# Kernel optimization log

Hardware: AMD Instinct MI355X
Metric: run time of the kernel (lower is better)

The kernel has to match this reference:

```python
import jax, jax.numpy as jnp
import numpy as np
import math

N, LQ, C = 4, 5440, 256
H, L, P = 8, 4, 4
D = C // H
SHAPES = [(64, 64), (32, 32), (16, 16), (8, 8)]
STARTS = [0, 4096, 5120, 5376]
LEN_IN = 5440


def setup_inputs() -> dict:
    key = jax.random.key(0)
    ks = jax.random.split(key, 12)
    s = 1.0 / math.sqrt(C)
    return {
        "query": jax.random.normal(ks[0], (N, LQ, C), jnp.float32),
        "reference_points": jax.random.uniform(ks[1], (N, LQ, L, 2), jnp.float32),
        "input_flatten": jax.random.normal(ks[2], (N, LEN_IN, C), jnp.float32),
        "input_spatial_shapes": jnp.asarray(SHAPES, jnp.int32),
        "input_level_start_index": jnp.asarray(STARTS, jnp.int32),
        "w_off": jax.random.normal(ks[3], (C, H * L * P * 2), jnp.float32) * 0.01,
        "b_off": jax.random.normal(ks[4], (H * L * P * 2,), jnp.float32) * 0.5,
        "w_attn": jax.random.normal(ks[5], (C, H * L * P), jnp.float32) * 0.01,
        "b_attn": jnp.zeros((H * L * P,), jnp.float32),
        "w_val": jax.random.normal(ks[6], (C, C), jnp.float32) * s,
        "b_val": jnp.zeros((C,), jnp.float32),
        "w_out": jax.random.normal(ks[7], (C, C), jnp.float32) * s,
        "b_out": jnp.zeros((C,), jnp.float32),
    }


def _gather_corner(lv, yi, xi, w):
    # lv: (N, h*w, H, D); yi, xi: (N, Lq, H, P) int32 -> (N, Lq, H, P, D)
    n, lq, h_, p_ = yi.shape
    idx = yi * w + xi
    idx2 = idx.transpose(0, 1, 3, 2).reshape(n, lq * p_, h_)[..., None]
    g = jnp.take_along_axis(lv, idx2, axis=1)  # (N, Lq*P, H, D)
    return g.reshape(n, lq, p_, h_, -1).transpose(0, 1, 3, 2, 4)


def _msdeform(query, reference_points, input_flatten, shapes, starts,
              w_off, b_off, w_attn, b_attn, w_val, b_val, w_out, b_out):
    n, lq, c = query.shape
    value = (input_flatten @ w_val + b_val).reshape(n, -1, H, D)
    off = (query @ w_off + b_off).reshape(n, lq, H, L, P, 2)
    attn = jax.nn.softmax((query @ w_attn + b_attn).reshape(n, lq, H, L * P), axis=-1)
    # sampling locations in [0,1], (N, Lq, H, L, P, 2)
    loc = jnp.clip(reference_points[:, :, None, :, None, :] + off, 0.0, 1.0)
    sampled = []
    for lvl, (hh, ww) in enumerate(shapes):
        s0 = starts[lvl]
        lv = value[:, s0:s0 + hh * ww]  # (N, hh*ww, H, D)
        xy = loc[:, :, :, lvl] * jnp.asarray([ww, hh], jnp.float32) - 0.5  # (N,Lq,H,P,2)
        x, y = xy[..., 0], xy[..., 1]
        x0 = jnp.floor(x)
        y0 = jnp.floor(y)
        x0i = jnp.clip(x0.astype(jnp.int32), 0, ww - 1)
        x1i = jnp.clip(x0.astype(jnp.int32) + 1, 0, ww - 1)
        y0i = jnp.clip(y0.astype(jnp.int32), 0, hh - 1)
        y1i = jnp.clip(y0.astype(jnp.int32) + 1, 0, hh - 1)
        x0f, x1f = x0i.astype(x.dtype), x1i.astype(x.dtype)
        y0f, y1f = y0i.astype(y.dtype), y1i.astype(y.dtype)
        wa = ((x1f - x) * (y1f - y))[..., None]
        wb = ((x1f - x) * (y - y0f))[..., None]
        wc = ((x - x0f) * (y1f - y))[..., None]
        wd = ((x - x0f) * (y - y0f))[..., None]
        va = _gather_corner(lv, y0i, x0i, ww)
        vb = _gather_corner(lv, y1i, x0i, ww)
        vc = _gather_corner(lv, y0i, x1i, ww)
        vd = _gather_corner(lv, y1i, x1i, ww)
        sampled.append(wa * va + wb * vb + wc * vc + wd * vd)
    sampled = jnp.concatenate(sampled, axis=3)  # (N, Lq, H, L*P, D)
    out = jnp.einsum('nqhp,nqhpd->nqhd', attn, sampled).reshape(n, lq, c)
    return out @ w_out + b_out


def reference(query, reference_points, input_flatten, input_spatial_shapes,
              input_level_start_index, w_off, b_off, w_attn, b_attn,
              w_val, b_val, w_out, b_out):
    shapes = [tuple(int(v) for v in row) for row in np.asarray(input_spatial_shapes)]
    starts = [int(v) for v in np.asarray(input_level_start_index)]
    return _msdeform(query, reference_points, input_flatten, shapes, starts,
                     w_off, b_off, w_attn, b_attn, w_val, b_val, w_out, b_out)
```

## Files before the change

kernel.cpp:

```cpp
#include <hip/hip_runtime.h>
#include <hip/hip_fp16.h>
#include <math.h>

#define C_DIM 256
#define H_DIM 8
#define L_DIM 4
#define P_DIM 4
#define LQ 5440
#define LEN_IN 5440
#define NB 4
#define M_ROWS (NB * LQ)
#define NPANEL (M_ROWS / 128)

typedef __attribute__((ext_vector_type(8))) _Float16 f16x8;
typedef __attribute__((ext_vector_type(8))) unsigned short u16x8;
typedef __attribute__((ext_vector_type(4))) float f32x4;

__device__ __forceinline__ void split_f32(float a, __half& h, __half& l) {
    h = __float2half(a);
    l = __float2half(a - __half2float(h));
}

__global__ __launch_bounds__(256) void convert_all(const float* __restrict__ w_val,
                                                   const float* __restrict__ w_off,
                                                   const float* __restrict__ w_attn,
                                                   const float* __restrict__ w_out,
                                                   const float* __restrict__ b_off,
                                                   const float* __restrict__ b_attn,
                                                   __half* __restrict__ wv_hi, __half* __restrict__ wv_lo,
                                                   __half* __restrict__ wc_hi, __half* __restrict__ wc_lo,
                                                   __half* __restrict__ wt_hi, __half* __restrict__ wt_lo,
                                                   float* __restrict__ bc) {
    const int b = blockIdx.x, k = threadIdx.x;
    if (b < 896) {
        const float* w; __half *hi, *lo; int ncols, col, orow;
        if (b < 256)      { w = w_val;  hi = wv_hi; lo = wv_lo; ncols = 256; col = b;       orow = col; }
        else if (b < 512) { w = w_off;  hi = wc_hi; lo = wc_lo; ncols = 256; col = b - 256; orow = col; }
        else if (b < 640) { w = w_attn; hi = wc_hi; lo = wc_lo; ncols = 128; col = b - 512; orow = col + 256; }
        else              { w = w_out;  hi = wt_hi; lo = wt_lo; ncols = 256; col = b - 640; orow = col; }
        const float a = w[(size_t)k * ncols + col];
        __half h, l;
        split_f32(a, h, l);
        hi[(size_t)orow * 256 + k] = h;
        lo[(size_t)orow * 256 + k] = l;
    } else if (b == 896) {
        bc[k] = b_off[k];
    } else {
        if (k < 128) bc[256 + k] = b_attn[k];
    }
}

template <int NC, int BN, int MINW>
__global__ __launch_bounds__(256, MINW) void gemm_f16x3(const float* __restrict__ A,
                                                        const __half* __restrict__ Bhi,
                                                        const __half* __restrict__ Blo,
                                                        const float* __restrict__ bias,
                                                        float* __restrict__ outp) {
    constexpr int NF = BN / 32;
    constexpr int BCH = BN / 64;
    constexpr int WC = BN / 2;
    constexpr int NCH = WC / 4;

    __shared__ __align__(16) __half sA[2][128][32];
    __shared__ __align__(16) __half sB[2][BN][32];
    __shared__ __align__(16) float sepi[4][16][WC];

    const int n0 = blockIdx.x * BN;
    const int row0 = blockIdx.y * 128;
    const int t = threadIdx.x;
    const int w = t >> 6, lane = t & 63;
    const int bm = (w >> 1) * 64, bn = (w & 1) * WC;
    const int fr = lane & 15;
    const int fc = lane >> 4;

    const int ar1 = t >> 2, ar2 = ar1 + 64;
    const int ak8 = t & 3;
    const int asw1 = (ak8 ^ ((ar1 >> 1) & 3)) * 8;
    const int asw2 = (ak8 ^ ((ar2 >> 1) & 3)) * 8;
    const int bc8 = t & 3;
    int brr[BCH], bsw[BCH];
#pragma unroll
    for (int cc = 0; cc < BCH; ++cc) {
        brr[cc] = (t >> 2) + 64 * cc;
        bsw[cc] = (bc8 ^ ((brr[cc] >> 1) & 3)) * 8;
    }

    const size_t ga1 = (size_t)(row0 + ar1) * 256 + ak8 * 8;
    const size_t ga2 = (size_t)(row0 + ar2) * 256 + ak8 * 8;
    size_t gb[BCH];
#pragma unroll
    for (int cc = 0; cc < BCH; ++cc) gb[cc] = (size_t)(n0 + brr[cc]) * 256 + bc8 * 8;

    f32x4 acc[4][NF];
#pragma unroll
    for (int m = 0; m < 4; ++m)
#pragma unroll
        for (int n = 0; n < NF; ++n)
#pragma unroll
            for (int r = 0; r < 4; ++r) acc[m][n][r] = 0.f;

    float4 pa[4];
    float4 pb[2 * BCH];
    pa[0] = *(const float4*)(A + ga1);
    pa[1] = *(const float4*)(A + ga1 + 4);
    pa[2] = *(const float4*)(A + ga2);
    pa[3] = *(const float4*)(A + ga2 + 4);
#pragma unroll
    for (int cc = 0; cc < BCH; ++cc) {
        pb[cc] = *(const float4*)(Bhi + gb[cc]);
        pb[BCH + cc] = *(const float4*)(Blo + gb[cc]);
    }

    for (int kt = 0; kt < 8; ++kt) {
        if (kt) __syncthreads();
#pragma unroll
        for (int ch = 0; ch < 2; ++ch) {
            const float4 u = pa[2 * ch], v = pa[2 * ch + 1];
            const float e[8] = {u.x, u.y, u.z, u.w, v.x, v.y, v.z, v.w};
            u16x8 Hh, Ll;
#pragma unroll
            for (int i = 0; i < 8; ++i) {
                __half h, l;
                split_f32(e[i], h, l);
                Hh[i] = __half_as_ushort(h);
                Ll[i] = __half_as_ushort(l);
            }
            const int row = ch ? ar2 : ar1;
            const int sw = ch ? asw2 : asw1;
            *(u16x8*)&sA[0][row][sw] = Hh;
            *(u16x8*)&sA[1][row][sw] = Ll;
        }
#pragma unroll
        for (int cc = 0; cc < BCH; ++cc) {
            *(float4*)&sB[0][brr[cc]][bsw[cc]] = pb[cc];
            *(float4*)&sB[1][brr[cc]][bsw[cc]] = pb[BCH + cc];
        }
        __syncthreads();
        if (kt < 7) {
            const size_t ko = (size_t)(kt + 1) * 32;
            pa[0] = *(const float4*)(A + ga1 + ko);
            pa[1] = *(const float4*)(A + ga1 + ko + 4);
            pa[2] = *(const float4*)(A + ga2 + ko);
            pa[3] = *(const float4*)(A + ga2 + ko + 4);
#pragma unroll
            for (int cc = 0; cc < BCH; ++cc) {
                pb[cc] = *(const float4*)(Bhi + gb[cc] + ko);
                pb[BCH + cc] = *(const float4*)(Blo + gb[cc] + ko);
            }
        }

        f16x8 bhf[NF], blf[NF];
#pragma unroll
        for (int n = 0; n < NF; ++n) {
            const int rowb = bn + n * 16 + fr;
            const int swb = (fc ^ ((rowb >> 1) & 3)) * 8;
            bhf[n] = *(const f16x8*)&sB[0][rowb][swb];
            blf[n] = *(const f16x8*)&sB[1][rowb][swb];
        }
#pragma unroll
        for (int m = 0; m < 4; ++m) {
            const int rowa = bm + m * 16 + fr;
            const int swa = (fc ^ ((rowa >> 1) & 3)) * 8;
            const f16x8 ah = *(const f16x8*)&sA[0][rowa][swa];
            const f16x8 al = *(const f16x8*)&sA[1][rowa][swa];
#pragma unroll
            for (int n = 0; n < NF; ++n) {
                acc[m][n] = __builtin_amdgcn_mfma_f32_16x16x32_f16(ah, bhf[n], acc[m][n], 0, 0, 0);
                acc[m][n] = __builtin_amdgcn_mfma_f32_16x16x32_f16(al, bhf[n], acc[m][n], 0, 0, 0);
                acc[m][n] = __builtin_amdgcn_mfma_f32_16x16x32_f16(ah, blf[n], acc[m][n], 0, 0, 0);
            }
        }
    }

    float bv[NF];
#pragma unroll
    for (int n = 0; n < NF; ++n) bv[n] = bias[n0 + bn + n * 16 + fr];

#pragma unroll
    for (int m = 0; m < 4; ++m) {
#pragma unroll
        for (int n = 0; n < NF; ++n) {
            const int kch = n * 4 + (fr >> 2);
            const int lo4 = fr & 3;
#pragma unroll
            for (int r = 0; r < 4; ++r) {
                const int rw = fc * 4 + r;
                const int sk = (kch ^ (rw & 7)) & (NCH - 1);
                sepi[w][rw][sk * 4 + lo4] = acc[m][n][r] + bv[n];
            }
        }
#pragma unroll
        for (int jj = 0; jj < NF; ++jj) {
            const int flat = jj * 64 + lane;
            const int rw = flat / NCH;
            const int k = flat % NCH;
            const int sk = (k ^ (rw & 7)) & (NCH - 1);
            const float4 vv = *(const float4*)&sepi[w][rw][sk * 4];
            const int grow = row0 + bm + m * 16 + rw;
            *(float4*)&outp[(size_t)grow * NC + (n0 + bn + k * 4)] = vv;
        }
    }
}

__global__ __launch_bounds__(256) void sample_kernel(const float* __restrict__ value,
                                                     const float* __restrict__ ol,
                                                     const float* __restrict__ refpts,
                                                     float* __restrict__ tmp) {
    const int t = threadIdx.x;
    const int w = t >> 6, lane = t & 63;

    __shared__ __align__(16) float4 s_aw[4][128];
    __shared__ __align__(16) uint4 s_of[4][128];

    const int h = lane >> 3;
    const unsigned l16 = (unsigned)(lane * 16);

    const int bid = blockIdx.x;
    const int xcd = bid & 7;
    const int pos = bid >> 3;
    const int n = xcd >> 1;
    const int qgrp = (xcd & 1) * 340 + pos;

    const char* vbn = (const char*)value + (size_t)n * (LEN_IN * C_DIM * 4);

    for (int it = 0; it < 2; ++it) {
        const int q = n * LQ + qgrp * 8 + w * 2 + it;

#pragma unroll
        for (int s = 0; s < 2; ++s) {
            const int j = lane + 64 * s;
            const int hq = j >> 4, lp = j & 15;
            const int l = lp >> 2;
            const int ww = 64 >> l;
            int st = 0;
            if (l == 1) st = 4096;
            else if (l == 2) st = 5120;
            else if (l == 3) st = 5376;

            const float2 oxy = *(const float2*)&ol[(size_t)q * 384 + 2 * j];
            const float2 rxy = *(const float2*)&refpts[((size_t)q * L_DIM + l) * 2];

            const float fw = (float)ww;
            const float x = fminf(fmaxf(rxy.x + oxy.x, 0.f), 1.f) * fw - 0.5f;
            const float y = fminf(fmaxf(rxy.y + oxy.y, 0.f), 1.f) * fw - 0.5f;
            const int xi = (int)floorf(x);
            const int yi = (int)floorf(y);
            const int x0i = min(max(xi, 0), ww - 1);
            const int x1i = min(max(xi + 1, 0), ww - 1);
            const int y0i = min(max(yi, 0), ww - 1);
            const int y1i = min(max(yi + 1, 0), ww - 1);
            const float wx0 = (float)x1i - x, wx1 = x - (float)x0i;
            const float wy0 = (float)y1i - y, wy1 = y - (float)y0i;

            const float lg = ol[(size_t)q * 384 + 256 + j];
            float m = lg;
#pragma unroll
            for (int o = 8; o; o >>= 1) m = fmaxf(m, __shfl_xor(m, o, 16));
            const float e = expf(lg - m);
            float sm = e;
#pragma unroll
            for (int o = 8; o; o >>= 1) sm += __shfl_xor(sm, o, 16);
            const float a = e / sm;

            const int p = lp * 8 + (hq ^ (lp & 7));
            float4 aw;
            aw.x = a * (wx0 * wy0);
            aw.y = a * (wx0 * wy1);
            aw.z = a * (wx1 * wy0);
            aw.w = a * (wx1 * wy1);
            uint4 of;
            of.x = (unsigned)(st + y0i * ww + x0i) << 10;
            of.y = (unsigned)(st + y1i * ww + x0i) << 10;
            of.z = (unsigned)(st + y0i * ww + x1i) << 10;
            of.w = (unsigned)(st + y1i * ww + x1i) << 10;
            s_aw[w][p] = aw;
            s_of[w][p] = of;
        }

        float4 acc;
        acc.x = 0.f; acc.y = 0.f; acc.z = 0.f; acc.w = 0.f;
#pragma unroll
        for (int lp = 0; lp < 16; ++lp) {
            const int p = lp * 8 + (h ^ (lp & 7));
            const float4 aw = s_aw[w][p];
            const uint4 of = s_of[w][p];
            const float4 v0 = *(const float4*)(vbn + (of.x + l16));
            const float4 v1 = *(const float4*)(vbn + (of.y + l16));
            const float4 v2 = *(const float4*)(vbn + (of.z + l16));
            const float4 v3 = *(const float4*)(vbn + (of.w + l16));
            acc.x += aw.x * v0.x + aw.y * v1.x + aw.z * v2.x + aw.w * v3.x;
            acc.y += aw.x * v0.y + aw.y * v1.y + aw.z * v2.y + aw.w * v3.y;
            acc.z += aw.x * v0.z + aw.y * v1.z + aw.z * v2.z + aw.w * v3.z;
            acc.w += aw.x * v0.w + aw.y * v1.w + aw.z * v2.w + aw.w * v3.w;
        }
        *(float4*)&tmp[(size_t)q * 256 + (size_t)(lane * 4)] = acc;
    }
}

extern "C" void kernel_launch(void* const* d_in, const int* in_sizes, int n_in,
                              void* d_out, int out_size, void* d_ws, size_t ws_size,
                              hipStream_t stream) {
    const float* query         = (const float*)d_in[0];
    const float* refpts        = (const float*)d_in[1];
    const float* input_flatten = (const float*)d_in[2];
    const float* w_off  = (const float*)d_in[5];
    const float* b_off  = (const float*)d_in[6];
    const float* w_attn = (const float*)d_in[7];
    const float* b_attn = (const float*)d_in[8];
    const float* w_val  = (const float*)d_in[9];
    const float* b_val  = (const float*)d_in[10];
    const float* w_out  = (const float*)d_in[11];
    const float* b_out  = (const float*)d_in[12];
    float* out = (float*)d_out;

    const size_t nr = (size_t)M_ROWS;
    float* p = (float*)d_ws;
    float* value_ws = p; p += nr * 256;
    float* ol_ws    = p; p += nr * 384;
    float* tmp_ws   = p; p += nr * 256;
    float* bc_ws    = p; p += 384;
    __half* wv_hi = (__half*)p;
    __half* wv_lo = wv_hi + 256 * 256;
    __half* wc_hi = wv_lo + 256 * 256;
    __half* wc_lo = wc_hi + 384 * 256;
    __half* wt_hi = wc_lo + 384 * 256;
    __half* wt_lo = wt_hi + 256 * 256;

    convert_all<<<898, 256, 0, stream>>>(w_val, w_off, w_attn, w_out, b_off, b_attn,
                                         wv_hi, wv_lo, wc_hi, wc_lo, wt_hi, wt_lo, bc_ws);

    dim3 g256(4, M_ROWS / 128);
    dim3 g384(3, M_ROWS / 128);

    gemm_f16x3<256, 64, 4><<<g256, 256, 0, stream>>>(input_flatten, wv_hi, wv_lo, b_val, value_ws);
    gemm_f16x3<384, 128, 2><<<g384, 256, 0, stream>>>(query, wc_hi, wc_lo, bc_ws, ol_ws);

    sample_kernel<<<M_ROWS / 8, 256, 0, stream>>>(value_ws, ol_ws, refpts, tmp_ws);

    gemm_f16x3<256, 64, 4><<<g256, 256, 0, stream>>>(tmp_ws, wt_hi, wt_lo, b_out, out);
}
```

Measured before the change: 138.6 us.

## Prefetch A two k-tiles ahead and remap GEMM blocks for XCD locality

The GEMM main loop is unrolled by two with separate register sets, so global loads of the A operand are issued two k-tiles ahead and have more time to cover memory latency. The 2D grid becomes a 1D grid whose block IDs are remapped so that blocks sharing a row panel are interleaved by groups of 8. This likely aims at L2 locality across the XCDs. The price is more registers held live, which may lower occupancy, and a few idle blocks that return early because the panel count is padded to 176.

```diff
diff --git a/kernel.cpp b/kernel.cpp
--- a/kernel.cpp
+++ b/kernel.cpp
@@ -50,6 +50,71 @@
     }
 }
 
+
+#define STAGE_A_CHUNK(U, V, ROW, SW)                                      \
+    {                                                                     \
+        const float e_[8] = {U.x, U.y, U.z, U.w, V.x, V.y, V.z, V.w};     \
+        u16x8 Hh_, Ll_;                                                   \
+        _Pragma("unroll")                                                 \
+        for (int i_ = 0; i_ < 8; ++i_) {                                  \
+            __half h_, l_;                                                \
+            split_f32(e_[i_], h_, l_);                                    \
+            Hh_[i_] = __half_as_ushort(h_);                               \
+            Ll_[i_] = __half_as_ushort(l_);                               \
+        }                                                                 \
+        *(u16x8*)&sA[0][ROW][SW] = Hh_;                                   \
+        *(u16x8*)&sA[1][ROW][SW] = Ll_;                                   \
+    }
+
+#define GEMM_PHASE(KT, P0, P1, P2, P3, PRE)                               \
+    {                                                                     \
+        if ((KT) > 0) __syncthreads();                                    \
+        STAGE_A_CHUNK(P0, P1, ar1, asw1);                                 \
+        STAGE_A_CHUNK(P2, P3, ar2, asw2);                                 \
+        _Pragma("unroll")                                                 \
+        for (int cc_ = 0; cc_ < BCH; ++cc_) {                             \
+            *(float4*)&sB[0][brr[cc_]][bsw[cc_]] = pb[cc_];               \
+            *(float4*)&sB[1][brr[cc_]][bsw[cc_]] = pb[BCH + cc_];         \
+        }                                                                 \
+        __syncthreads();                                                  \
+        if ((PRE) < 8) {                                                  \
+            const size_t ko_ = (size_t)(PRE) * 32;                        \
+            P0 = *(const float4*)(A + ga1 + ko_);                         \
+            P1 = *(const float4*)(A + ga1 + ko_ + 4);                     \
+            P2 = *(const float4*)(A + ga2 + ko_);                         \
+            P3 = *(const float4*)(A + ga2 + ko_ + 4);                     \
+        }                                                                 \
+        if ((KT) + 1 < 8) {                                               \
+            const size_t kb_ = (size_t)((KT) + 1) * 32;                   \
+            _Pragma("unroll")                                             \
+            for (int cc_ = 0; cc_ < BCH; ++cc_) {                         \
+                pb[cc_] = *(const float4*)(Bhi + gb[cc_] + kb_);          \
+                pb[BCH + cc_] = *(const float4*)(Blo + gb[cc_] + kb_);    \
+            }                                                             \
+        }                                                                 \
+        f16x8 bhf_[NF], blf_[NF];                                         \
+        _Pragma("unroll")                                                 \
+        for (int n_ = 0; n_ < NF; ++n_) {                                 \
+            const int rowb_ = bn + n_ * 16 + fr;                          \
+            const int swb_ = (fc ^ ((rowb_ >> 1) & 3)) * 8;               \
+            bhf_[n_] = *(const f16x8*)&sB[0][rowb_][swb_];                \
+            blf_[n_] = *(const f16x8*)&sB[1][rowb_][swb_];                \
+        }                                                                 \
+        _Pragma("unroll")                                                 \
+        for (int m_ = 0; m_ < 4; ++m_) {                                  \
+            const int rowa_ = bm + m_ * 16 + fr;                          \
+            const int swa_ = (fc ^ ((rowa_ >> 1) & 3)) * 8;               \
+            const f16x8 ah_ = *(const f16x8*)&sA[0][rowa_][swa_];         \
+            const f16x8 al_ = *(const f16x8*)&sA[1][rowa_][swa_];         \
+            _Pragma("unroll")                                             \
+            for (int n_ = 0; n_ < NF; ++n_) {                             \
+                acc[m_][n_] = __builtin_amdgcn_mfma_f32_16x16x32_f16(ah_, bhf_[n_], acc[m_][n_], 0, 0, 0); \
+                acc[m_][n_] = __builtin_amdgcn_mfma_f32_16x16x32_f16(al_, bhf_[n_], acc[m_][n_], 0, 0, 0); \
+                acc[m_][n_] = __builtin_amdgcn_mfma_f32_16x16x32_f16(ah_, blf_[n_], acc[m_][n_], 0, 0, 0); \
+            }                                                             \
+        }                                                                 \
+    }
+
 template <int NC, int BN, int MINW>
 __global__ __launch_bounds__(256, MINW) void gemm_f16x3(const float* __restrict__ A,
                                                         const __half* __restrict__ Bhi,
@@ -60,13 +125,22 @@
     constexpr int BCH = BN / 64;
     constexpr int WC = BN / 2;
     constexpr int NCH = WC / 4;
+    constexpr int NX = NC / BN;
 
     __shared__ __align__(16) __half sA[2][128][32];
     __shared__ __align__(16) __half sB[2][BN][32];
     __shared__ __align__(16) float sepi[4][16][WC];
 
-    const int n0 = blockIdx.x * BN;
-    const int row0 = blockIdx.y * 128;
+    const int bid = blockIdx.x;
+    const int c = bid & 7;
+    const int rest = bid >> 3;
+    const int x = rest % NX;
+    const int yg = rest / NX;
+    const int y = yg * 8 + c;
+    if (y >= NPANEL) return;
+
+    const int n0 = x * BN;
+    const int row0 = y * 128;
     const int t = threadIdx.x;
     const int w = t >> 6, lane = t & 63;
     const int bm = (w >> 1) * 64, bn = (w & 1) * WC;
@@ -99,77 +173,24 @@
 #pragma unroll
             for (int r = 0; r < 4; ++r) acc[m][n][r] = 0.f;
 
-    float4 pa[4];
+    float4 pa0 = *(const float4*)(A + ga1);
+    float4 pa1 = *(const float4*)(A + ga1 + 4);
+    float4 pa2 = *(const float4*)(A + ga2);
+    float4 pa3 = *(const float4*)(A + ga2 + 4);
     float4 pb[2 * BCH];
-    pa[0] = *(const float4*)(A + ga1);
-    pa[1] = *(const float4*)(A + ga1 + 4);
-    pa[2] = *(const float4*)(A + ga2);
-    pa[3] = *(const float4*)(A + ga2 + 4);
 #pragma unroll
     for (int cc = 0; cc < BCH; ++cc) {
         pb[cc] = *(const float4*)(Bhi + gb[cc]);
         pb[BCH + cc] = *(const float4*)(Blo + gb[cc]);
     }
-
-    for (int kt = 0; kt < 8; ++kt) {
-        if (kt) __syncthreads();
-#pragma unroll
-        for (int ch = 0; ch < 2; ++ch) {
-            const float4 u = pa[2 * ch], v = pa[2 * ch + 1];
-            const float e[8] = {u.x, u.y, u.z, u.w, v.x, v.y, v.z, v.w};
-            u16x8 Hh, Ll;
-#pragma unroll
-            for (int i = 0; i < 8; ++i) {
-                __half h, l;
-                split_f32(e[i], h, l);
-                Hh[i] = __half_as_ushort(h);
-                Ll[i] = __half_as_ushort(l);
-            }
-            const int row = ch ? ar2 : ar1;
-            const int sw = ch ? asw2 : asw1;
-            *(u16x8*)&sA[0][row][sw] = Hh;
-            *(u16x8*)&sA[1][row][sw] = Ll;
-        }
-#pragma unroll
-        for (int cc = 0; cc < BCH; ++cc) {
-            *(float4*)&sB[0][brr[cc]][bsw[cc]] = pb[cc];
-            *(float4*)&sB[1][brr[cc]][bsw[cc]] = pb[BCH + cc];
-        }
-        __syncthreads();
-        if (kt < 7) {
-            const size_t ko = (size_t)(kt + 1) * 32;
-            pa[0] = *(const float4*)(A + ga1 + ko);
-            pa[1] = *(const float4*)(A + ga1 + ko + 4);
-            pa[2] = *(const float4*)(A + ga2 + ko);
-            pa[3] = *(const float4*)(A + ga2 + ko + 4);
-#pragma unroll
-            for (int cc = 0; cc < BCH; ++cc) {
-                pb[cc] = *(const float4*)(Bhi + gb[cc] + ko);
-                pb[BCH + cc] = *(const float4*)(Blo + gb[cc] + ko);
-            }
-        }
-
-        f16x8 bhf[NF], blf[NF];
-#pragma unroll
-        for (int n = 0; n < NF; ++n) {
-            const int rowb = bn + n * 16 + fr;
-            const int swb = (fc ^ ((rowb >> 1) & 3)) * 8;
-            bhf[n] = *(const f16x8*)&sB[0][rowb][swb];
-            blf[n] = *(const f16x8*)&sB[1][rowb][swb];
-        }
-#pragma unroll
-        for (int m = 0; m < 4; ++m) {
-            const int rowa = bm + m * 16 + fr;
-            const int swa = (fc ^ ((rowa >> 1) & 3)) * 8;
-            const f16x8 ah = *(const f16x8*)&sA[0][rowa][swa];
-            const f16x8 al = *(const f16x8*)&sA[1][rowa][swa];
-#pragma unroll
-            for (int n = 0; n < NF; ++n) {
-                acc[m][n] = __builtin_amdgcn_mfma_f32_16x16x32_f16(ah, bhf[n], acc[m][n], 0, 0, 0);
-                acc[m][n] = __builtin_amdgcn_mfma_f32_16x16x32_f16(al, bhf[n], acc[m][n], 0, 0, 0);
-                acc[m][n] = __builtin_amdgcn_mfma_f32_16x16x32_f16(ah, blf[n], acc[m][n], 0, 0, 0);
-            }
-        }
+    float4 qa0 = *(const float4*)(A + ga1 + 32);
+    float4 qa1 = *(const float4*)(A + ga1 + 36);
+    float4 qa2 = *(const float4*)(A + ga2 + 32);
+    float4 qa3 = *(const float4*)(A + ga2 + 36);
+
+    for (int kt2 = 0; kt2 < 8; kt2 += 2) {
+        GEMM_PHASE(kt2, pa0, pa1, pa2, pa3, kt2 + 2);
+        GEMM_PHASE(kt2 + 1, qa0, qa1, qa2, qa3, kt2 + 3);
     }
 
     float bv[NF];
@@ -329,8 +350,8 @@
     convert_all<<<898, 256, 0, stream>>>(w_val, w_off, w_attn, w_out, b_off, b_attn,
                                          wv_hi, wv_lo, wc_hi, wc_lo, wt_hi, wt_lo, bc_ws);
 
-    dim3 g256(4, M_ROWS / 128);
-    dim3 g384(3, M_ROWS / 128);
+    const int g256 = 8 * 4 * 22;
+    const int g384 = 8 * 3 * 22;
 
     gemm_f16x3<256, 64, 4><<<g256, 256, 0, stream>>>(input_flatten, wv_hi, wv_lo, b_val, value_ws);
     gemm_f16x3<384, 128, 2><<<g384, 256, 0, stream>>>(query, wc_hi, wc_lo, bc_ws, ol_ws);
```

Result: slower. 148.1 us (+6.8%).
